# Kernel optimization log

Measured on AMD Instinct MI355X. Metric: run time of the kernel, lower is better.

## Reference

```python
import jax, jax.numpy as jnp
import numpy as np

H, W, C = 64, 64, 2048
IMG = 224


def setup_inputs() -> dict:
    key = jax.random.key(0)
    features = jax.random.normal(key, (2, H, W, C), dtype=jnp.float32)
    return {"features": features, "img_size": IMG}


def reference(features, img_size):
    # features: [2, H, W, C] -- query (index 0) and target (index 1) feature maps.
    x0 = features[0]  # [H, W, C]
    x1 = features[1]  # [H, W, C]
    # Correlation volume: Decomposition[i,j,k,l] = sum_c x0[i,j,c] * x1[k,l,c]
    # (replaces the quadruple Python loop with a single GEMM-shaped einsum)
    decom = jnp.einsum('ijc,klc->ijkl', x0, x1)  # [H, W, H, W]
    decom = decom / jnp.max(decom)
    # NOTE: source calls `Decomposition.clamp(min=0)` without assignment -> no-op.
    decom_1 = jnp.sum(decom, axis=(2, 3))  # [H, W] saliency on query image
    decom_2 = jnp.sum(decom, axis=(0, 1))  # [H, W] saliency on target image
    stacked = jnp.stack((decom_1, decom_2))  # [2, H, W]
    # F.interpolate(mode='bilinear', align_corners=False) == half-pixel bilinear resize
    out = jax.image.resize(stacked, (2, img_size, img_size), method='bilinear')
    return out  # [2, img_size, img_size]
```

## Files before the change

kernel.cpp:

```cpp
#include <hip/hip_runtime.h>
#include <hip/hip_bf16.h>

#define HW    4096
#define CDIM  2048
#define IMG   224
#define NTKI  64
#define NTM   128
#define LROW  528
#define QSCALE 21.166666f
#define NS    32

typedef int   int4v  __attribute__((ext_vector_type(4)));
typedef int   i32x16 __attribute__((ext_vector_type(16)));
typedef char  char4v __attribute__((ext_vector_type(4)));

__device__ __forceinline__ i32x16 zi16() {
    i32x16 z;
#pragma unroll
    for (int i = 0; i < 16; ++i) z[i] = 0;
    return z;
}
__device__ __forceinline__ char quant8(float x) {
    int r = __float2int_rn(x * QSCALE);
    r = min(max(r, -127), 127);
    return (char)r;
}

__device__ __forceinline__ void gload_lds16(const char* g, char* l) {
    __builtin_amdgcn_global_load_lds(
        (const __attribute__((address_space(1))) void*)g,
        (__attribute__((address_space(3))) void*)l, 16, 0, 0);
}

__global__ __launch_bounds__(256) void convert_pack_partial(
    const float* __restrict__ feat,
    char* __restrict__ Ap, char* __restrict__ Bp,
    float* __restrict__ P) {
    __shared__ char lds[64 * LROW];
    __shared__ float csum[512];
    const int tid = threadIdx.x;
    const int mat = blockIdx.z;
    const int rm  = blockIdx.y;
    const int kb0 = blockIdx.x * 512;
    const float* src = feat + (size_t)mat * HW * CDIM + (size_t)(rm * 64) * CDIM + kb0;

    const int cc = (tid & 127) * 4;
    float a0 = 0.f, a1 = 0.f, a2 = 0.f, a3 = 0.f;
#pragma unroll
    for (int j = 0; j < 32; ++j) {
        const int r = j * 2 + (tid >> 7);
        float4 v = *(const float4*)&src[(size_t)r * CDIM + cc];
        a0 += v.x; a1 += v.y; a2 += v.z; a3 += v.w;
        char4v q;
        q[0] = quant8(v.x); q[1] = quant8(v.y);
        q[2] = quant8(v.z); q[3] = quant8(v.w);
        *(char4v*)&lds[r * LROW + cc] = q;
    }
    if (tid >= 128) {
        csum[cc + 0] = a0; csum[cc + 1] = a1;
        csum[cc + 2] = a2; csum[cc + 3] = a3;
    }
    __syncthreads();
    if (tid < 128) {
        float4 p;
        p.x = a0 + csum[cc + 0]; p.y = a1 + csum[cc + 1];
        p.z = a2 + csum[cc + 2]; p.w = a3 + csum[cc + 3];
        *(float4*)&P[((size_t)mat * 64 + rm) * CDIM + kb0 + cc] = p;
    }

    const int l = tid & 63, w = tid >> 6;
    char* dstbase = mat ? Bp : Ap;
#pragma unroll
    for (int i = 0; i < 8; ++i) {
        const int t = w * 8 + i;
        const int tml = t >> 4, tkl = t & 15;
        int4v v = *(const int4v*)
            &lds[(tml * 32 + (l & 31)) * LROW + tkl * 32 + (l >> 5) * 16];
        const int tm  = rm * 2 + tml;
        const int tkg = blockIdx.x * 16 + tkl;
        *(int4v*)&dstbase[((size_t)(tm * NTKI + tkg) * 64 + l) * 16] = v;
    }
}

__global__ __launch_bounds__(512, 2) void gemm_max_kernel(
    const char* __restrict__ Ap, const char* __restrict__ Bp,
    const float* __restrict__ P, float* __restrict__ s,
    float* __restrict__ blockmax) {
    __shared__ char lds[4 * 32768];
    __shared__ int wred[8];
    const int tid  = threadIdx.x;
    const int lane = tid & 63;
    const int wave = tid >> 6;
    const int wm = wave >> 2, wn = wave & 3;
    const int bm = blockIdx.y, bn = blockIdx.x;

    const char* gb[4];
    int loff[4];
#pragma unroll
    for (int q = 0; q < 4; ++q) {
        const int c = wave * 4 + q;
        const int kk = c & 1;
        if (c < 16) {
            const int il = c >> 1;
            gb[q] = Ap + ((size_t)(bm * 8 + il) * NTKI + kk) * 1024 + lane * 16;
            loff[q] = (il * 2 + kk) * 1024;
        } else {
            const int jl = (c - 16) >> 1;
            gb[q] = Bp + ((size_t)(bn * 8 + jl) * NTKI + kk) * 1024 + lane * 16;
            loff[q] = 16384 + (jl * 2 + kk) * 1024;
        }
    }

#define ISSUE_STAGE(S) do {                                         \
        char* buf_ = lds + (((S) & 3) << 15);                       \
        _Pragma("unroll")                                           \
        for (int q = 0; q < 4; ++q)                                 \
            gload_lds16(gb[q] + (size_t)(S) * 2048, buf_ + loff[q]);\
    } while (0)
#define ISSUE_HALF(S, Q0) do {                                      \
        char* buf_ = lds + (((S) & 3) << 15);                       \
        gload_lds16(gb[Q0]     + (size_t)(S) * 2048, buf_ + loff[Q0]);     \
        gload_lds16(gb[Q0 + 1] + (size_t)(S) * 2048, buf_ + loff[Q0 + 1]); \
    } while (0)

    ISSUE_STAGE(0); ISSUE_STAGE(1); ISSUE_STAGE(2);

    if (bm == 0 && bn < 16 && tid < 256) {
        const int gc = bn * 256 + tid;
        const float* Pp = P + (size_t)(gc >> 11) * 64 * CDIM + (gc & 2047);
        float sum = 0.f;
#pragma unroll 8
        for (int r = 0; r < 64; ++r) sum += Pp[(size_t)r * CDIM];
        s[gc] = sum;
    }

    asm volatile("s_waitcnt vmcnt(8)" ::: "memory");
    asm volatile("s_barrier" ::: "memory");

    const int abase = wm * 8192 + lane * 16;
    const int bbase = 16384 + wn * 4096 + lane * 16;

    i32x16 acc00 = zi16(), acc01 = zi16();
    i32x16 acc10 = zi16(), acc11 = zi16();
    i32x16 acc20 = zi16(), acc21 = zi16();
    i32x16 acc30 = zi16(), acc31 = zi16();

    for (int st = 0; st < NS; ++st) {
        const char* ab = lds + ((st & 3) << 15) + abase;
        const char* bb = lds + ((st & 3) << 15) + bbase;

        {
            int4v a0 = *(const int4v*)(ab);
            int4v a1 = *(const int4v*)(ab + 2048);
            int4v a2 = *(const int4v*)(ab + 4096);
            int4v a3 = *(const int4v*)(ab + 6144);
            int4v b0 = *(const int4v*)(bb);
            int4v b1 = *(const int4v*)(bb + 2048);
            if (st + 3 < NS) ISSUE_HALF(st + 3, 0);
            asm volatile("s_barrier" ::: "memory");
            asm volatile("s_waitcnt lgkmcnt(0)" ::: "memory");
            __builtin_amdgcn_s_setprio(1);
            acc00 = __builtin_amdgcn_mfma_i32_32x32x32_i8(a0, b0, acc00, 0, 0, 0);
            acc01 = __builtin_amdgcn_mfma_i32_32x32x32_i8(a0, b1, acc01, 0, 0, 0);
            acc10 = __builtin_amdgcn_mfma_i32_32x32x32_i8(a1, b0, acc10, 0, 0, 0);
            acc11 = __builtin_amdgcn_mfma_i32_32x32x32_i8(a1, b1, acc11, 0, 0, 0);
            acc20 = __builtin_amdgcn_mfma_i32_32x32x32_i8(a2, b0, acc20, 0, 0, 0);
            acc21 = __builtin_amdgcn_mfma_i32_32x32x32_i8(a2, b1, acc21, 0, 0, 0);
            acc30 = __builtin_amdgcn_mfma_i32_32x32x32_i8(a3, b0, acc30, 0, 0, 0);
            acc31 = __builtin_amdgcn_mfma_i32_32x32x32_i8(a3, b1, acc31, 0, 0, 0);
            __builtin_amdgcn_s_setprio(0);
            asm volatile("s_barrier" ::: "memory");
        }

        {
            int4v a0 = *(const int4v*)(ab + 1024);
            int4v a1 = *(const int4v*)(ab + 2048 + 1024);
            int4v a2 = *(const int4v*)(ab + 4096 + 1024);
            int4v a3 = *(const int4v*)(ab + 6144 + 1024);
            int4v b0 = *(const int4v*)(bb + 1024);
            int4v b1 = *(const int4v*)(bb + 2048 + 1024);
            if (st + 3 < NS) ISSUE_HALF(st + 3, 2);
            if (st < NS - 3)       { asm volatile("s_waitcnt vmcnt(8)" ::: "memory"); }
            else if (st == NS - 3) { asm volatile("s_waitcnt vmcnt(4)" ::: "memory"); }
            else if (st == NS - 2) { asm volatile("s_waitcnt vmcnt(0)" ::: "memory"); }
            asm volatile("s_barrier" ::: "memory");
            asm volatile("s_waitcnt lgkmcnt(0)" ::: "memory");
            __builtin_amdgcn_s_setprio(1);
            acc00 = __builtin_amdgcn_mfma_i32_32x32x32_i8(a0, b0, acc00, 0, 0, 0);
            acc01 = __builtin_amdgcn_mfma_i32_32x32x32_i8(a0, b1, acc01, 0, 0, 0);
            acc10 = __builtin_amdgcn_mfma_i32_32x32x32_i8(a1, b0, acc10, 0, 0, 0);
            acc11 = __builtin_amdgcn_mfma_i32_32x32x32_i8(a1, b1, acc11, 0, 0, 0);
            acc20 = __builtin_amdgcn_mfma_i32_32x32x32_i8(a2, b0, acc20, 0, 0, 0);
            acc21 = __builtin_amdgcn_mfma_i32_32x32x32_i8(a2, b1, acc21, 0, 0, 0);
            acc30 = __builtin_amdgcn_mfma_i32_32x32x32_i8(a3, b0, acc30, 0, 0, 0);
            acc31 = __builtin_amdgcn_mfma_i32_32x32x32_i8(a3, b1, acc31, 0, 0, 0);
            __builtin_amdgcn_s_setprio(0);
            asm volatile("s_barrier" ::: "memory");
        }
    }
#undef ISSUE_STAGE
#undef ISSUE_HALF

    int m = INT_MIN;
#pragma unroll
    for (int i = 0; i < 16; ++i) {
        m = max(m, acc00[i]); m = max(m, acc01[i]);
        m = max(m, acc10[i]); m = max(m, acc11[i]);
        m = max(m, acc20[i]); m = max(m, acc21[i]);
        m = max(m, acc30[i]); m = max(m, acc31[i]);
    }
#pragma unroll
    for (int off = 32; off; off >>= 1)
        m = max(m, __shfl_down(m, off));
    if (lane == 0) wred[wave] = m;
    __syncthreads();
    if (tid == 0) {
        int im = wred[0];
#pragma unroll
        for (int w2 = 1; w2 < 8; ++w2) im = max(im, wred[w2]);
        blockmax[blockIdx.y * gridDim.x + blockIdx.x] =
            (float)im * (1.0f / (QSCALE * QSCALE));
    }
}

__global__ __launch_bounds__(256) void saliency_kernel(
    const float* __restrict__ feat, const float* __restrict__ s,
    float* __restrict__ sal) {
    const int tid = threadIdx.x, lane = tid & 63, wave = tid >> 6;
    const int g = blockIdx.x * 4 + wave;
    const float* x;
    const float* sv;
    if (g < HW) { x = feat + (size_t)g * CDIM;                            sv = s + CDIM; }
    else        { x = feat + (size_t)HW * CDIM + (size_t)(g - HW) * CDIM; sv = s; }
    float acc = 0.f;
#pragma unroll
    for (int it = 0; it < 8; ++it) {
        const int c0 = it * 256 + lane * 4;
        float4 v = *(const float4*)&x[c0];
        float4 w = *(const float4*)&sv[c0];
        acc += v.x * w.x + v.y * w.y + v.z * w.z + v.w * w.w;
    }
#pragma unroll
    for (int off = 32; off; off >>= 1) acc += __shfl_down(acc, off);
    if (lane == 0) sal[g] = acc;
}

__global__ __launch_bounds__(256) void resize_kernel(
    const float* __restrict__ sal, const float* __restrict__ bmax,
    float* __restrict__ out) {
    __shared__ float w[4];
    __shared__ float rM;
    const int tid = threadIdx.x;
    float m = -3.4e38f;
    for (int i = tid; i < 256; i += 256) m = fmaxf(m, bmax[i]);
#pragma unroll
    for (int off = 32; off; off >>= 1) m = fmaxf(m, __shfl_down(m, off));
    if ((tid & 63) == 0) w[tid >> 6] = m;
    __syncthreads();
    if (tid == 0)
        rM = 1.0f / fmaxf(fmaxf(w[0], w[1]), fmaxf(w[2], w[3]));
    __syncthreads();

    const int idx = blockIdx.x * 256 + tid;
    if (idx >= 2 * IMG * IMG) return;
    const int ch = idx / (IMG * IMG);
    const int rem = idx % (IMG * IMG);
    const int oy = rem / IMG, ox = rem % IMG;
    const float scale = 64.0f / (float)IMG;
    const float sy = ((float)oy + 0.5f) * scale - 0.5f;
    const float sx = ((float)ox + 0.5f) * scale - 0.5f;
    const float fy0 = floorf(sy), fx0 = floorf(sx);
    const float wy = sy - fy0, wx = sx - fx0;
    int y0 = (int)fy0, x0 = (int)fx0;
    int y1 = min(max(y0 + 1, 0), 63), x1 = min(max(x0 + 1, 0), 63);
    y0 = min(max(y0, 0), 63); x0 = min(max(x0, 0), 63);
    const float* p = sal + ch * HW;
    const float v00 = p[y0 * 64 + x0], v01 = p[y0 * 64 + x1];
    const float v10 = p[y1 * 64 + x0], v11 = p[y1 * 64 + x1];
    out[idx] = ((1.f - wy) * ((1.f - wx) * v00 + wx * v01) +
                wy * ((1.f - wx) * v10 + wx * v11)) * rM;
}

extern "C" void kernel_launch(void* const* d_in, const int* in_sizes, int n_in,
                              void* d_out, int out_size, void* d_ws, size_t ws_size,
                              hipStream_t stream) {
    const float* feat = (const float*)d_in[0];
    float* out = (float*)d_out;

    char* ws = (char*)d_ws;
    char* Ap = ws;
    char* Bp = ws + (size_t)8 * 1024 * 1024;
    float* P    = (float*)(ws + (size_t)16 * 1024 * 1024);
    float* s    = P + 2 * 64 * CDIM;
    float* bmax = s + 2 * CDIM;
    float* sal  = bmax + 1024;

    convert_pack_partial<<<dim3(4, 64, 2), 256, 0, stream>>>(feat, Ap, Bp, P);
    gemm_max_kernel<<<dim3(16, 16), 512, 0, stream>>>(Ap, Bp, P, s, bmax);
    saliency_kernel<<<2048, 256, 0, stream>>>(feat, s, sal);
    const int nout = 2 * IMG * IMG;
    resize_kernel<<<(nout + 255) / 256, 256, 0, stream>>>(sal, bmax, out);
}
```

Measured before the change: 139.9 us.

## Fuse four kernels into one cooperative persistent kernel with grid syncs

Replaces the convert/pack, int8 GEMM-max, saliency and resize launches with a single cooperative kernel of 256 blocks that steps through the phases, separated by grid.sync. This removes three kernel launch boundaries and the tail gaps between them. In exchange, the convert and saliency phases now run on only 256 blocks with fixed work per block instead of wide grids, which may lower memory parallelism. It also requires every block to be co-resident for the cooperative launch.

```diff
diff --git a/kernel.cpp b/kernel.cpp
--- a/kernel.cpp
+++ b/kernel.cpp
@@ -1,11 +1,12 @@
 #include <hip/hip_runtime.h>
-#include <hip/hip_bf16.h>
+#include <hip/hip_cooperative_groups.h>
+
+namespace cg = cooperative_groups;
 
 #define HW    4096
 #define CDIM  2048
 #define IMG   224
 #define NTKI  64
-#define NTM   128
 #define LROW  528
 #define QSCALE 21.166666f
 #define NS    32
@@ -25,91 +26,102 @@
     r = min(max(r, -127), 127);
     return (char)r;
 }
-
 __device__ __forceinline__ void gload_lds16(const char* g, char* l) {
     __builtin_amdgcn_global_load_lds(
         (const __attribute__((address_space(1))) void*)g,
         (__attribute__((address_space(3))) void*)l, 16, 0, 0);
 }
 
-__global__ __launch_bounds__(256) void convert_pack_partial(
+__global__ __launch_bounds__(512, 2) void simcam_fused(
     const float* __restrict__ feat,
     char* __restrict__ Ap, char* __restrict__ Bp,
-    float* __restrict__ P) {
-    __shared__ char lds[64 * LROW];
-    __shared__ float csum[512];
-    const int tid = threadIdx.x;
-    const int mat = blockIdx.z;
-    const int rm  = blockIdx.y;
-    const int kb0 = blockIdx.x * 512;
-    const float* src = feat + (size_t)mat * HW * CDIM + (size_t)(rm * 64) * CDIM + kb0;
-
-    const int cc = (tid & 127) * 4;
-    float a0 = 0.f, a1 = 0.f, a2 = 0.f, a3 = 0.f;
-#pragma unroll
-    for (int j = 0; j < 32; ++j) {
-        const int r = j * 2 + (tid >> 7);
-        float4 v = *(const float4*)&src[(size_t)r * CDIM + cc];
-        a0 += v.x; a1 += v.y; a2 += v.z; a3 += v.w;
-        char4v q;
-        q[0] = quant8(v.x); q[1] = quant8(v.y);
-        q[2] = quant8(v.z); q[3] = quant8(v.w);
-        *(char4v*)&lds[r * LROW + cc] = q;
-    }
-    if (tid >= 128) {
-        csum[cc + 0] = a0; csum[cc + 1] = a1;
-        csum[cc + 2] = a2; csum[cc + 3] = a3;
-    }
-    __syncthreads();
-    if (tid < 128) {
-        float4 p;
-        p.x = a0 + csum[cc + 0]; p.y = a1 + csum[cc + 1];
-        p.z = a2 + csum[cc + 2]; p.w = a3 + csum[cc + 3];
-        *(float4*)&P[((size_t)mat * 64 + rm) * CDIM + kb0 + cc] = p;
-    }
-
-    const int l = tid & 63, w = tid >> 6;
-    char* dstbase = mat ? Bp : Ap;
-#pragma unroll
-    for (int i = 0; i < 8; ++i) {
-        const int t = w * 8 + i;
-        const int tml = t >> 4, tkl = t & 15;
-        int4v v = *(const int4v*)
-            &lds[(tml * 32 + (l & 31)) * LROW + tkl * 32 + (l >> 5) * 16];
-        const int tm  = rm * 2 + tml;
-        const int tkg = blockIdx.x * 16 + tkl;
-        *(int4v*)&dstbase[((size_t)(tm * NTKI + tkg) * 64 + l) * 16] = v;
-    }
-}
-
-__global__ __launch_bounds__(512, 2) void gemm_max_kernel(
-    const char* __restrict__ Ap, const char* __restrict__ Bp,
-    const float* __restrict__ P, float* __restrict__ s,
-    float* __restrict__ blockmax) {
-    __shared__ char lds[4 * 32768];
+    float* __restrict__ P, float* __restrict__ s,
+    float* __restrict__ blockmax, float* __restrict__ sal,
+    float* __restrict__ out) {
+    __shared__ char smem[131072];
     __shared__ int wred[8];
+    __shared__ float wmax8[8];
+    __shared__ float rM;
+    cg::grid_group grid = cg::this_grid();
+
     const int tid  = threadIdx.x;
+    const int bid  = blockIdx.x;
     const int lane = tid & 63;
     const int wave = tid >> 6;
-    const int wm = wave >> 2, wn = wave & 3;
-    const int bm = blockIdx.y, bn = blockIdx.x;
-
-    const char* gb[4];
-    int loff[4];
-#pragma unroll
-    for (int q = 0; q < 4; ++q) {
-        const int c = wave * 4 + q;
-        const int kk = c & 1;
-        if (c < 16) {
-            const int il = c >> 1;
-            gb[q] = Ap + ((size_t)(bm * 8 + il) * NTKI + kk) * 1024 + lane * 16;
-            loff[q] = (il * 2 + kk) * 1024;
-        } else {
-            const int jl = (c - 16) >> 1;
-            gb[q] = Bp + ((size_t)(bn * 8 + jl) * NTKI + kk) * 1024 + lane * 16;
-            loff[q] = 16384 + (jl * 2 + kk) * 1024;
+
+    {
+        const int h = tid >> 8;
+        const int t = tid & 255;
+        const int u = bid * 2 + h;
+        const int kb  = u >> 7;
+        const int rm  = (u >> 1) & 63;
+        const int mat = u & 1;
+        char*  tile = smem + h * 33792;
+        float* csum = (float*)(smem + 67584) + (h << 9);
+        const int kb0 = kb * 512;
+        const float* src = feat + (size_t)mat * HW * CDIM
+                         + (size_t)(rm * 64) * CDIM + kb0;
+
+        const int cc = (t & 127) * 4;
+        float a0 = 0.f, a1 = 0.f, a2 = 0.f, a3 = 0.f;
+#pragma unroll
+        for (int j = 0; j < 32; ++j) {
+            const int r = j * 2 + (t >> 7);
+            float4 v = *(const float4*)&src[(size_t)r * CDIM + cc];
+            a0 += v.x; a1 += v.y; a2 += v.z; a3 += v.w;
+            char4v q;
+            q[0] = quant8(v.x); q[1] = quant8(v.y);
+            q[2] = quant8(v.z); q[3] = quant8(v.w);
+            *(char4v*)&tile[r * LROW + cc] = q;
+        }
+        if (t >= 128) {
+            csum[cc + 0] = a0; csum[cc + 1] = a1;
+            csum[cc + 2] = a2; csum[cc + 3] = a3;
+        }
+        __syncthreads();
+        if (t < 128) {
+            float4 p;
+            p.x = a0 + csum[cc + 0]; p.y = a1 + csum[cc + 1];
+            p.z = a2 + csum[cc + 2]; p.w = a3 + csum[cc + 3];
+            *(float4*)&P[((size_t)mat * 64 + rm) * CDIM + kb0 + cc] = p;
+        }
+        const int l = t & 63, w = t >> 6;
+        char* dstbase = mat ? Bp : Ap;
+#pragma unroll
+        for (int i = 0; i < 8; ++i) {
+            const int t2  = w * 8 + i;
+            const int tml = t2 >> 4, tkl = t2 & 15;
+            int4v v = *(const int4v*)
+                &tile[(tml * 32 + (l & 31)) * LROW + tkl * 32 + (l >> 5) * 16];
+            const int tm  = rm * 2 + tml;
+            const int tkg = kb * 16 + tkl;
+            *(int4v*)&dstbase[((size_t)(tm * NTKI + tkg) * 64 + l) * 16] = v;
         }
     }
+
+    grid.sync();
+
+    {
+        char* lds = smem;
+        const int wm = wave >> 2, wn = wave & 3;
+        const int bm = bid >> 4, bn = bid & 15;
+
+        const char* gb[4];
+        int loff[4];
+#pragma unroll
+        for (int q = 0; q < 4; ++q) {
+            const int c = wave * 4 + q;
+            const int kk = c & 1;
+            if (c < 16) {
+                const int il = c >> 1;
+                gb[q] = Ap + ((size_t)(bm * 8 + il) * NTKI + kk) * 1024 + lane * 16;
+                loff[q] = (il * 2 + kk) * 1024;
+            } else {
+                const int jl = (c - 16) >> 1;
+                gb[q] = Bp + ((size_t)(bn * 8 + jl) * NTKI + kk) * 1024 + lane * 16;
+                loff[q] = 16384 + (jl * 2 + kk) * 1024;
+            }
+        }
 
 #define ISSUE_STAGE(S) do {                                         \
         char* buf_ = lds + (((S) & 3) << 15);                       \
@@ -123,162 +135,160 @@
         gload_lds16(gb[Q0 + 1] + (size_t)(S) * 2048, buf_ + loff[Q0 + 1]); \
     } while (0)
 
-    ISSUE_STAGE(0); ISSUE_STAGE(1); ISSUE_STAGE(2);
-
-    if (bm == 0 && bn < 16 && tid < 256) {
-        const int gc = bn * 256 + tid;
-        const float* Pp = P + (size_t)(gc >> 11) * 64 * CDIM + (gc & 2047);
-        float sum = 0.f;
+        ISSUE_STAGE(0); ISSUE_STAGE(1); ISSUE_STAGE(2);
+
+        if (bid < 16 && tid < 256) {
+            const int gc = bid * 256 + tid;
+            const float* Pp = P + (size_t)(gc >> 11) * 64 * CDIM + (gc & 2047);
+            float sum = 0.f;
 #pragma unroll 8
-        for (int r = 0; r < 64; ++r) sum += Pp[(size_t)r * CDIM];
-        s[gc] = sum;
-    }
-
-    asm volatile("s_waitcnt vmcnt(8)" ::: "memory");
-    asm volatile("s_barrier" ::: "memory");
-
-    const int abase = wm * 8192 + lane * 16;
-    const int bbase = 16384 + wn * 4096 + lane * 16;
-
-    i32x16 acc00 = zi16(), acc01 = zi16();
-    i32x16 acc10 = zi16(), acc11 = zi16();
-    i32x16 acc20 = zi16(), acc21 = zi16();
-    i32x16 acc30 = zi16(), acc31 = zi16();
-
-    for (int st = 0; st < NS; ++st) {
-        const char* ab = lds + ((st & 3) << 15) + abase;
-        const char* bb = lds + ((st & 3) << 15) + bbase;
-
-        {
-            int4v a0 = *(const int4v*)(ab);
-            int4v a1 = *(const int4v*)(ab + 2048);
-            int4v a2 = *(const int4v*)(ab + 4096);
-            int4v a3 = *(const int4v*)(ab + 6144);
-            int4v b0 = *(const int4v*)(bb);
-            int4v b1 = *(const int4v*)(bb + 2048);
-            if (st + 3 < NS) ISSUE_HALF(st + 3, 0);
-            asm volatile("s_barrier" ::: "memory");
-            asm volatile("s_waitcnt lgkmcnt(0)" ::: "memory");
-            __builtin_amdgcn_s_setprio(1);
-            acc00 = __builtin_amdgcn_mfma_i32_32x32x32_i8(a0, b0, acc00, 0, 0, 0);
-            acc01 = __builtin_amdgcn_mfma_i32_32x32x32_i8(a0, b1, acc01, 0, 0, 0);
-            acc10 = __builtin_amdgcn_mfma_i32_32x32x32_i8(a1, b0, acc10, 0, 0, 0);
-            acc11 = __builtin_amdgcn_mfma_i32_32x32x32_i8(a1, b1, acc11, 0, 0, 0);
-            acc20 = __builtin_amdgcn_mfma_i32_32x32x32_i8(a2, b0, acc20, 0, 0, 0);
-            acc21 = __builtin_amdgcn_mfma_i32_32x32x32_i8(a2, b1, acc21, 0, 0, 0);
-            acc30 = __builtin_amdgcn_mfma_i32_32x32x32_i8(a3, b0, acc30, 0, 0, 0);
-            acc31 = __builtin_amdgcn_mfma_i32_32x32x32_i8(a3, b1, acc31, 0, 0, 0);
-            __builtin_amdgcn_s_setprio(0);
-            asm volatile("s_barrier" ::: "memory");
-        }
-
-        {
-            int4v a0 = *(const int4v*)(ab + 1024);
-            int4v a1 = *(const int4v*)(ab + 2048 + 1024);
-            int4v a2 = *(const int4v*)(ab + 4096 + 1024);
-            int4v a3 = *(const int4v*)(ab + 6144 + 1024);
-            int4v b0 = *(const int4v*)(bb + 1024);
-            int4v b1 = *(const int4v*)(bb + 2048 + 1024);
-            if (st + 3 < NS) ISSUE_HALF(st + 3, 2);
-            if (st < NS - 3)       { asm volatile("s_waitcnt vmcnt(8)" ::: "memory"); }
-            else if (st == NS - 3) { asm volatile("s_waitcnt vmcnt(4)" ::: "memory"); }
-            else if (st == NS - 2) { asm volatile("s_waitcnt vmcnt(0)" ::: "memory"); }
-            asm volatile("s_barrier" ::: "memory");
-            asm volatile("s_waitcnt lgkmcnt(0)" ::: "memory");
-            __builtin_amdgcn_s_setprio(1);
-            acc00 = __builtin_amdgcn_mfma_i32_32x32x32_i8(a0, b0, acc00, 0, 0, 0);
-            acc01 = __builtin_amdgcn_mfma_i32_32x32x32_i8(a0, b1, acc01, 0, 0, 0);
-            acc10 = __builtin_amdgcn_mfma_i32_32x32x32_i8(a1, b0, acc10, 0, 0, 0);
-            acc11 = __builtin_amdgcn_mfma_i32_32x32x32_i8(a1, b1, acc11, 0, 0, 0);
-            acc20 = __builtin_amdgcn_mfma_i32_32x32x32_i8(a2, b0, acc20, 0, 0, 0);
-            acc21 = __builtin_amdgcn_mfma_i32_32x32x32_i8(a2, b1, acc21, 0, 0, 0);
-            acc30 = __builtin_amdgcn_mfma_i32_32x32x32_i8(a3, b0, acc30, 0, 0, 0);
-            acc31 = __builtin_amdgcn_mfma_i32_32x32x32_i8(a3, b1, acc31, 0, 0, 0);
-            __builtin_amdgcn_s_setprio(0);
-            asm volatile("s_barrier" ::: "memory");
-        }
-    }
+            for (int r = 0; r < 64; ++r) sum += Pp[(size_t)r * CDIM];
+            s[gc] = sum;
+        }
+
+        asm volatile("s_waitcnt vmcnt(8)" ::: "memory");
+        asm volatile("s_barrier" ::: "memory");
+
+        const int abase = wm * 8192 + lane * 16;
+        const int bbase = 16384 + wn * 4096 + lane * 16;
+
+        i32x16 acc00 = zi16(), acc01 = zi16();
+        i32x16 acc10 = zi16(), acc11 = zi16();
+        i32x16 acc20 = zi16(), acc21 = zi16();
+        i32x16 acc30 = zi16(), acc31 = zi16();
+
+#define MM(i, j, A, B) acc##i##j = __builtin_amdgcn_mfma_i32_32x32x32_i8(A, B, acc##i##j, 0, 0, 0)
+
+        for (int st = 0; st < NS; ++st) {
+            const char* ab = lds + ((st & 3) << 15) + abase;
+            const char* bb = lds + ((st & 3) << 15) + bbase;
+
+            {
+                int4v a0 = *(const int4v*)(ab);
+                int4v a1 = *(const int4v*)(ab + 2048);
+                int4v a2 = *(const int4v*)(ab + 4096);
+                int4v a3 = *(const int4v*)(ab + 6144);
+                int4v b0 = *(const int4v*)(bb);
+                int4v b1 = *(const int4v*)(bb + 2048);
+                if (st + 3 < NS) ISSUE_HALF(st + 3, 0);
+                asm volatile("s_barrier" ::: "memory");
+                asm volatile("s_waitcnt lgkmcnt(0)" ::: "memory");
+                __builtin_amdgcn_s_setprio(1);
+                MM(0,0,a0,b0); MM(0,1,a0,b1);
+                MM(1,0,a1,b0); MM(1,1,a1,b1);
+                MM(2,0,a2,b0); MM(2,1,a2,b1);
+                MM(3,0,a3,b0); MM(3,1,a3,b1);
+                __builtin_amdgcn_s_setprio(0);
+                asm volatile("s_barrier" ::: "memory");
+            }
+            {
+                int4v a0 = *(const int4v*)(ab + 1024);
+                int4v a1 = *(const int4v*)(ab + 2048 + 1024);
+                int4v a2 = *(const int4v*)(ab + 4096 + 1024);
+                int4v a3 = *(const int4v*)(ab + 6144 + 1024);
+                int4v b0 = *(const int4v*)(bb + 1024);
+                int4v b1 = *(const int4v*)(bb + 2048 + 1024);
+                if (st + 3 < NS) ISSUE_HALF(st + 3, 2);
+                if (st < NS - 3)       { asm volatile("s_waitcnt vmcnt(8)" ::: "memory"); }
+                else if (st == NS - 3) { asm volatile("s_waitcnt vmcnt(4)" ::: "memory"); }
+                else if (st == NS - 2) { asm volatile("s_waitcnt vmcnt(0)" ::: "memory"); }
+                asm volatile("s_barrier" ::: "memory");
+                asm volatile("s_waitcnt lgkmcnt(0)" ::: "memory");
+                __builtin_amdgcn_s_setprio(1);
+                MM(0,0,a0,b0); MM(0,1,a0,b1);
+                MM(1,0,a1,b0); MM(1,1,a1,b1);
+                MM(2,0,a2,b0); MM(2,1,a2,b1);
+                MM(3,0,a3,b0); MM(3,1,a3,b1);
+                __builtin_amdgcn_s_setprio(0);
+                asm volatile("s_barrier" ::: "memory");
+            }
+        }
 #undef ISSUE_STAGE
 #undef ISSUE_HALF
-
-    int m = INT_MIN;
-#pragma unroll
-    for (int i = 0; i < 16; ++i) {
-        m = max(m, acc00[i]); m = max(m, acc01[i]);
-        m = max(m, acc10[i]); m = max(m, acc11[i]);
-        m = max(m, acc20[i]); m = max(m, acc21[i]);
-        m = max(m, acc30[i]); m = max(m, acc31[i]);
+#undef MM
+
+        int m = INT_MIN;
+#pragma unroll
+        for (int i = 0; i < 16; ++i) {
+            m = max(m, acc00[i]); m = max(m, acc01[i]);
+            m = max(m, acc10[i]); m = max(m, acc11[i]);
+            m = max(m, acc20[i]); m = max(m, acc21[i]);
+            m = max(m, acc30[i]); m = max(m, acc31[i]);
+        }
+#pragma unroll
+        for (int off = 32; off; off >>= 1)
+            m = max(m, __shfl_down(m, off));
+        if (lane == 0) wred[wave] = m;
+        __syncthreads();
+        if (tid == 0) {
+            int im = wred[0];
+#pragma unroll
+            for (int w2 = 1; w2 < 8; ++w2) im = max(im, wred[w2]);
+            blockmax[bid] = (float)im * (1.0f / (QSCALE * QSCALE));
+        }
     }
-#pragma unroll
-    for (int off = 32; off; off >>= 1)
-        m = max(m, __shfl_down(m, off));
-    if (lane == 0) wred[wave] = m;
-    __syncthreads();
-    if (tid == 0) {
-        int im = wred[0];
-#pragma unroll
-        for (int w2 = 1; w2 < 8; ++w2) im = max(im, wred[w2]);
-        blockmax[blockIdx.y * gridDim.x + blockIdx.x] =
-            (float)im * (1.0f / (QSCALE * QSCALE));
+
+    grid.sync();
+
+    {
+#pragma unroll
+        for (int rr = 0; rr < 4; ++rr) {
+            const int g = bid * 32 + wave * 4 + rr;
+            const float* x;
+            const float* sv;
+            if (g < HW) { x = feat + (size_t)g * CDIM;                            sv = s + CDIM; }
+            else        { x = feat + (size_t)HW * CDIM + (size_t)(g - HW) * CDIM; sv = s; }
+            float a = 0.f;
+#pragma unroll
+            for (int it2 = 0; it2 < 8; ++it2) {
+                const int c0 = it2 * 256 + lane * 4;
+                float4 v  = *(const float4*)&x[c0];
+                float4 w2 = *(const float4*)&sv[c0];
+                a += v.x * w2.x + v.y * w2.y + v.z * w2.z + v.w * w2.w;
+            }
+#pragma unroll
+            for (int off = 32; off; off >>= 1) a += __shfl_down(a, off);
+            if (lane == 0) sal[g] = a;
+        }
     }
-}
-
-__global__ __launch_bounds__(256) void saliency_kernel(
-    const float* __restrict__ feat, const float* __restrict__ s,
-    float* __restrict__ sal) {
-    const int tid = threadIdx.x, lane = tid & 63, wave = tid >> 6;
-    const int g = blockIdx.x * 4 + wave;
-    const float* x;
-    const float* sv;
-    if (g < HW) { x = feat + (size_t)g * CDIM;                            sv = s + CDIM; }
-    else        { x = feat + (size_t)HW * CDIM + (size_t)(g - HW) * CDIM; sv = s; }
-    float acc = 0.f;
-#pragma unroll
-    for (int it = 0; it < 8; ++it) {
-        const int c0 = it * 256 + lane * 4;
-        float4 v = *(const float4*)&x[c0];
-        float4 w = *(const float4*)&sv[c0];
-        acc += v.x * w.x + v.y * w.y + v.z * w.z + v.w * w.w;
+
+    grid.sync();
+
+    {
+        float m = -3.4e38f;
+        if (tid < 256) m = blockmax[tid];
+#pragma unroll
+        for (int off = 32; off; off >>= 1) m = fmaxf(m, __shfl_down(m, off));
+        if (lane == 0) wmax8[wave] = m;
+        __syncthreads();
+        if (tid == 0) {
+            float mm = wmax8[0];
+#pragma unroll
+            for (int w2 = 1; w2 < 8; ++w2) mm = fmaxf(mm, wmax8[w2]);
+            rM = 1.0f / mm;
+        }
+        __syncthreads();
+
+        const int idx = bid * 512 + tid;
+        if (idx < 2 * IMG * IMG) {
+            const int ch  = idx / (IMG * IMG);
+            const int rem = idx % (IMG * IMG);
+            const int oy = rem / IMG, ox = rem % IMG;
+            const float scale = 64.0f / (float)IMG;
+            const float sy = ((float)oy + 0.5f) * scale - 0.5f;
+            const float sx = ((float)ox + 0.5f) * scale - 0.5f;
+            const float fy0 = floorf(sy), fx0 = floorf(sx);
+            const float wy = sy - fy0, wx = sx - fx0;
+            int y0 = (int)fy0, x0 = (int)fx0;
+            int y1 = min(max(y0 + 1, 0), 63), x1 = min(max(x0 + 1, 0), 63);
+            y0 = min(max(y0, 0), 63); x0 = min(max(x0, 0), 63);
+            const float* p = sal + ch * HW;
+            const float v00 = p[y0 * 64 + x0], v01 = p[y0 * 64 + x1];
+            const float v10 = p[y1 * 64 + x0], v11 = p[y1 * 64 + x1];
+            out[idx] = ((1.f - wy) * ((1.f - wx) * v00 + wx * v01) +
+                        wy * ((1.f - wx) * v10 + wx * v11)) * rM;
+        }
     }
-#pragma unroll
-    for (int off = 32; off; off >>= 1) acc += __shfl_down(acc, off);
-    if (lane == 0) sal[g] = acc;
-}
-
-__global__ __launch_bounds__(256) void resize_kernel(
-    const float* __restrict__ sal, const float* __restrict__ bmax,
-    float* __restrict__ out) {
-    __shared__ float w[4];
-    __shared__ float rM;
-    const int tid = threadIdx.x;
-    float m = -3.4e38f;
-    for (int i = tid; i < 256; i += 256) m = fmaxf(m, bmax[i]);
-#pragma unroll
-    for (int off = 32; off; off >>= 1) m = fmaxf(m, __shfl_down(m, off));
-    if ((tid & 63) == 0) w[tid >> 6] = m;
-    __syncthreads();
-    if (tid == 0)
-        rM = 1.0f / fmaxf(fmaxf(w[0], w[1]), fmaxf(w[2], w[3]));
-    __syncthreads();
-
-    const int idx = blockIdx.x * 256 + tid;
-    if (idx >= 2 * IMG * IMG) return;
-    const int ch = idx / (IMG * IMG);
-    const int rem = idx % (IMG * IMG);
-    const int oy = rem / IMG, ox = rem % IMG;
-    const float scale = 64.0f / (float)IMG;
-    const float sy = ((float)oy + 0.5f) * scale - 0.5f;
-    const float sx = ((float)ox + 0.5f) * scale - 0.5f;
-    const float fy0 = floorf(sy), fx0 = floorf(sx);
-    const float wy = sy - fy0, wx = sx - fx0;
-    int y0 = (int)fy0, x0 = (int)fx0;
-    int y1 = min(max(y0 + 1, 0), 63), x1 = min(max(x0 + 1, 0), 63);
-    y0 = min(max(y0, 0), 63); x0 = min(max(x0, 0), 63);
-    const float* p = sal + ch * HW;
-    const float v00 = p[y0 * 64 + x0], v01 = p[y0 * 64 + x1];
-    const float v10 = p[y1 * 64 + x0], v11 = p[y1 * 64 + x1];
-    out[idx] = ((1.f - wy) * ((1.f - wx) * v00 + wx * v01) +
-                wy * ((1.f - wx) * v10 + wx * v11)) * rM;
 }
 
 extern "C" void kernel_launch(void* const* d_in, const int* in_sizes, int n_in,
@@ -295,9 +305,8 @@
     float* bmax = s + 2 * CDIM;
     float* sal  = bmax + 1024;
 
-    convert_pack_partial<<<dim3(4, 64, 2), 256, 0, stream>>>(feat, Ap, Bp, P);
-    gemm_max_kernel<<<dim3(16, 16), 512, 0, stream>>>(Ap, Bp, P, s, bmax);
-    saliency_kernel<<<2048, 256, 0, stream>>>(feat, s, sal);
-    const int nout = 2 * IMG * IMG;
-    resize_kernel<<<(nout + 255) / 256, 256, 0, stream>>>(sal, bmax, out);
-}
+    void* kargs[] = { (void*)&feat, (void*)&Ap, (void*)&Bp, (void*)&P,
+                      (void*)&s, (void*)&bmax, (void*)&sal, (void*)&out };
+    hipLaunchCooperativeKernel((const void*)simcam_fused,
+                               dim3(256), dim3(512), kargs, 0, stream);
+}
```

New measurement: 245.2 us. 1.75x slower.
